# Kernel optimization log

Hardware: AMD Instinct MI355X
Metric: run time of the kernel (lower is better)

## Reference

```python
import jax, jax.numpy as jnp
import numpy as np
from jax.scipy.special import logsumexp

OT_ITER = 8
USE_POSITIVITY = True
LN_EPS = 1e-5
PROB_L = 2
EPS = 1e-4


def _layer_norm(x, w, b):
    mu = jnp.mean(x, axis=-1, keepdims=True)
    var = jnp.mean(jnp.square(x - mu), axis=-1, keepdims=True)
    return (x - mu) * jax.lax.rsqrt(var + LN_EPS) * w + b


def _sinkhorn(attn, log_mu, log_nu):
    # attn: [B, H, W+1, W+1]
    v = log_nu - logsumexp(attn, axis=2)
    u = log_mu - logsumexp(attn + v[:, :, None, :], axis=3)

    def step(uv, _):
        u, v = uv
        v = log_nu - logsumexp(attn + u[..., None], axis=2)
        u = log_mu - logsumexp(attn + v[:, :, None, :], axis=3)
        return (u, v), None

    (u, v), _ = jax.lax.scan(step, (u, v), None, length=OT_ITER - 1)
    return attn + u[..., None] + v[:, :, None, :]


def _optimal_transport(attn):
    w = attn.shape[-1]
    # pad one dustbin row/col with zeros
    attn = jnp.pad(attn, ((0, 0), (0, 0), (0, 1), (0, 1)))
    marginal = jnp.concatenate([jnp.ones((w,), attn.dtype), jnp.full((1,), float(w), attn.dtype)]) / (2.0 * w)
    log_mu = jnp.log(marginal).reshape(1, 1, w + 1)
    log_nu = log_mu
    out = _sinkhorn(attn, log_mu, log_nu)
    return jnp.exp(out[:, :, :-1, :-1] + jnp.log(2.0 * w))


def _forward(feature, ln_weight, ln_bias):
    w = feature.shape[-1]
    x = jnp.transpose(feature, (0, 2, 3, 1))          # [2B, H, W, C]
    x = _layer_norm(x, ln_weight, ln_bias)
    b2 = x.shape[0]
    f0, f1 = x[: b2 // 2], x[b2 // 2:]                 # [B, H, W, C] each

    cv = jnp.einsum('bhic,bhjc->bhij', f0, f1)         # [B, H, W, W]
    # F.interpolate(scale_factor=1/2, mode='nearest') == stride-2 slicing
    f0d, f1d = f0[:, ::2, ::2, :], f1[:, ::2, ::2, :]
    cv_down = jnp.einsum('bhic,bhjc->bhij', f0d, f1d)  # [B, H/2, W/2, W/2]

    if USE_POSITIVITY:
        mask = jnp.triu(jnp.ones((w, w), bool), 1)
    else:
        mask = jnp.zeros((w, w), bool)
    cv_mask = jnp.where(mask, -jnp.inf, cv)

    prob = _optimal_transport(cv_mask)                 # [B, H, W, W]
    masked_prob = jnp.where(mask, 0.0, prob)

    prob_max_ind = jnp.argmax(masked_prob, axis=-1)[..., None]  # [B, H, W, 1]
    mpp = jnp.pad(masked_prob, ((0, 0), (0, 0), (0, 0), (PROB_L, PROB_L)))

    conf = jnp.zeros_like(prob_max_ind, dtype=masked_prob.dtype)
    corr = jnp.zeros_like(conf)
    for idx in range(2 * PROB_L + 1):
        weight = jnp.take_along_axis(mpp, prob_max_ind + idx, axis=-1)
        conf = conf + weight
        corr = corr + weight * (prob_max_ind + idx - PROB_L).astype(weight.dtype)
    corr = (corr + EPS) / (conf + EPS)                 # [B, H, W, 1]

    x_grid = jnp.arange(w, dtype=feature.dtype)
    disparity = (x_grid[None, None, :] - corr[..., 0])[:, None]  # [B, 1, H, W]
    conf_out = conf[..., 0][:, None]                              # [B, 1, H, W]
    occ = jnp.sum(masked_prob, axis=-1)[:, None]                  # [B, 1, H, W]
    return (disparity, conf_out, occ, cv, cv_down)


def setup_inputs() -> dict:
    key = jax.random.key(0)
    k1, k2, k3 = jax.random.split(key, 3)
    feature = jax.random.normal(k1, (8, 128, 80, 256), jnp.float32)  # [2B, C, H, W]
    ln_weight = 1.0 + 0.02 * jax.random.normal(k2, (128,), jnp.float32)
    ln_bias = 0.02 * jax.random.normal(k3, (128,), jnp.float32)
    return {"feature": feature, "ln_weight": ln_weight, "ln_bias": ln_bias}


def reference(feature, ln_weight, ln_bias):
    return _forward(feature, ln_weight, ln_bias)
```

## Files before the change

kernel.cpp:

```cpp
#include <hip/hip_runtime.h>

#define CC 128
#define HH 80
#define WW 256
#define NSL 320
#define TRI2_TOT 36864
#define DISP_OFF 0
#define CONF_OFF 81920
#define OCC_OFF  163840
#define CV_OFF   245760
#define CVD_OFF  21217280
#define NU_C (1.0f/512.0f)
#define MU_C (1.0f/512.0f)
#define ST_N 163840
#define LDSW 40

typedef _Float16 f16;
typedef f16 f16x8 __attribute__((ext_vector_type(8)));
typedef float f32x4 __attribute__((ext_vector_type(4)));

__device__ __forceinline__ int ell_of(int m) { return 4 + (((m + 7) >> 3) << 5); }
__device__ __forceinline__ int S_of(int i) {
  int m = i >> 2;
  int q = (m + 7) >> 3, r = (m + 7) & 7;
  int Q = 16*m + ((q*(q-1)) << 9) + ((r*q) << 7);
  return Q + (i & 3) * ell_of(m);
}

__global__ __launch_bounds__(256)
void ln_stats_kernel(const float* __restrict__ feat, float* __restrict__ stats) {
  __shared__ __align__(16) float4 psum[8][32];
  __shared__ __align__(16) float4 psq[8][32];
  const int t = threadIdx.x;
  const int id = blockIdx.x;
  const int wx = id & 1, bh = id >> 1;
  const int bb = bh / HH, h = bh % HH;
  const int tw = t & 31, tc = t >> 5;
  const float* p = feat + ((size_t)(bb*CC + tc*16)*HH + h)*WW + wx*128 + tw*4;
  float4 s4  = make_float4(0.f, 0.f, 0.f, 0.f);
  float4 s24 = make_float4(0.f, 0.f, 0.f, 0.f);
  #pragma unroll
  for (int cc = 0; cc < 16; ++cc) {
    float4 v = *(const float4*)(p + (size_t)cc*HH*WW);
    s4.x += v.x; s4.y += v.y; s4.z += v.z; s4.w += v.w;
    s24.x = fmaf(v.x, v.x, s24.x); s24.y = fmaf(v.y, v.y, s24.y);
    s24.z = fmaf(v.z, v.z, s24.z); s24.w = fmaf(v.w, v.w, s24.w);
  }
  psum[tc][tw] = s4; psq[tc][tw] = s24;
  __syncthreads();
  if (t < 32) {
    float4 S  = psum[0][t];
    float4 S2 = psq[0][t];
    #pragma unroll
    for (int k = 1; k < 8; ++k) {
      float4 a = psum[k][t], b = psq[k][t];
      S.x += a.x; S.y += a.y; S.z += a.z; S.w += a.w;
      S2.x += b.x; S2.y += b.y; S2.z += b.z; S2.w += b.w;
    }
    float4 mu = make_float4(S.x*(1.f/CC), S.y*(1.f/CC), S.z*(1.f/CC), S.w*(1.f/CC));
    float4 rs;
    rs.x = rsqrtf(fmaf(-mu.x, mu.x, S2.x*(1.f/CC)) + 1e-5f);
    rs.y = rsqrtf(fmaf(-mu.y, mu.y, S2.y*(1.f/CC)) + 1e-5f);
    rs.z = rsqrtf(fmaf(-mu.z, mu.z, S2.z*(1.f/CC)) + 1e-5f);
    rs.w = rsqrtf(fmaf(-mu.w, mu.w, S2.w*(1.f/CC)) + 1e-5f);
    *(float4*)&stats[(size_t)bh*WW + wx*128 + 4*t]        = mu;
    *(float4*)&stats[ST_N + (size_t)bh*WW + wx*128 + 4*t] = rs;
  }
}

__global__ __launch_bounds__(256, 3)
void cv_fused_kernel(const float* __restrict__ feat, const float* __restrict__ stats,
                     const float* __restrict__ lnw, const float* __restrict__ lnb,
                     float* __restrict__ cv_out, float* __restrict__ cvd_out) {
  extern __shared__ unsigned short smu[];
  unsigned short* Ah = smu;
  unsigned short* Al = smu + 5120;
  unsigned short* Bh = smu + 10240;
  unsigned short* Bl = smu + 15360;
  __shared__ __align__(16) float rmean[256];
  __shared__ __align__(16) float rrstd[256];
  __shared__ float lwS[128], lbS[128];
  const int t = threadIdx.x;
  const int P = blockIdx.x;
  if (t < 128) { lwS[t] = lnw[t]; lbS[t] = lnb[t]; }
  const int l = t & 63, w = t >> 6;
  const int wm = w >> 1, wn = w & 1;
  const int fr = l & 15, fg = l >> 4;
  const int row = t & 127, khalf = t >> 7;

  const bool iscv = (P < 4*NSL);
  int zz = 0, i0 = 0, j0 = 0, id = 0, ws = 1;
  size_t baseA, baseB;
  if (iscv) {
    const int x = P & 7, m = P >> 3;
    const int q = m & 3, zhi = m >> 2;
    zz = zhi*8 + x;
    i0 = (q >> 1) * 128; j0 = (q & 1) * 128;
    const int b = zz / HH, h = zz % HH;
    baseA = ((size_t)b*CC*HH + (size_t)h)*WW + i0;
    baseB = ((size_t)(b+4)*CC*HH + (size_t)h)*WW + j0;
    const int isA = (t < 128);
    const int rr_ = isA ? (i0 + t) : (j0 + (t - 128));
    const int bb  = isA ? b : (b + 4);
    const size_t si = ((size_t)bb*HH + h)*WW + rr_;
    rmean[t] = stats[si];
    rrstd[t] = stats[ST_N + si];
  } else {
    id = P - 4*NSL;
    const int b = id / 40, hd = id % 40, h = 2*hd;
    ws = 2;
    baseA = ((size_t)b*CC*HH + (size_t)h)*WW;
    baseB = ((size_t)(b+4)*CC*HH + (size_t)h)*WW;
    const int isA = (t < 128);
    const int rowd = isA ? t : (t - 128);
    const int bb = isA ? b : (b + 4);
    const size_t si = ((size_t)bb*HH + h)*WW + 2*rowd;
    rmean[t] = stats[si];
    rrstd[t] = stats[ST_N + si];
  }

  f32x4 acc[4][4];
  #pragma unroll
  for (int mi = 0; mi < 4; ++mi)
    #pragma unroll
    for (int ni = 0; ni < 4; ++ni)
      acc[mi][ni] = (f32x4){0.f, 0.f, 0.f, 0.f};

  float qa[16], qb[16];
  auto loadC = [&](int kc) {
    const size_t co = (size_t)(kc*32 + khalf*16)*HH*WW + (size_t)(row*ws);
    #pragma unroll
    for (int e = 0; e < 16; ++e) {
      qa[e] = feat[baseA + co + (size_t)e*HH*WW];
      qb[e] = feat[baseB + co + (size_t)e*HH*WW];
    }
  };
  auto storeC = [&](int kc) {
    const float rmA = rmean[row],     rrA = rrstd[row];
    const float rmB = rmean[128+row], rrB = rrstd[128+row];
    f16x8 vah[2], val[2], vbh[2], vbl[2];
    #pragma unroll
    for (int e = 0; e < 16; ++e) {
      const int ch = kc*32 + khalf*16 + e;
      const float lw = lwS[ch], lb = lbS[ch];
      float va = (qa[e] - rmA) * rrA * lw + lb;
      f16 ha = (f16)va;
      vah[e >> 3][e & 7] = ha;
      val[e >> 3][e & 7] = (f16)(va - (float)ha);
      float vb = (qb[e] - rmB) * rrB * lw + lb;
      f16 hb = (f16)vb;
      vbh[e >> 3][e & 7] = hb;
      vbl[e >> 3][e & 7] = (f16)(vb - (float)hb);
    }
    const int off = row*LDSW + khalf*16;
    *(f16x8*)&Ah[off] = vah[0]; *(f16x8*)&Ah[off + 8] = vah[1];
    *(f16x8*)&Al[off] = val[0]; *(f16x8*)&Al[off + 8] = val[1];
    *(f16x8*)&Bh[off] = vbh[0]; *(f16x8*)&Bh[off + 8] = vbh[1];
    *(f16x8*)&Bl[off] = vbl[0]; *(f16x8*)&Bl[off + 8] = vbl[1];
  };
  auto compute = [&]() {
    f16x8 a_h[4], a_l[4];
    #pragma unroll
    for (int mi = 0; mi < 4; ++mi) {
      const int r0 = (wm*64 + mi*16 + fr)*LDSW + fg*8;
      a_h[mi] = *(const f16x8*)&Ah[r0];
      a_l[mi] = *(const f16x8*)&Al[r0];
    }
    #pragma unroll
    for (int ni = 0; ni < 4; ++ni) {
      const int c0 = (wn*64 + ni*16 + fr)*LDSW + fg*8;
      f16x8 b_h = *(const f16x8*)&Bh[c0];
      f16x8 b_l = *(const f16x8*)&Bl[c0];
      #pragma unroll
      for (int mi = 0; mi < 4; ++mi) {
        acc[mi][ni] = __builtin_amdgcn_mfma_f32_16x16x32_f16(a_h[mi], b_h, acc[mi][ni], 0, 0, 0);
        acc[mi][ni] = __builtin_amdgcn_mfma_f32_16x16x32_f16(a_h[mi], b_l, acc[mi][ni], 0, 0, 0);
        acc[mi][ni] = __builtin_amdgcn_mfma_f32_16x16x32_f16(a_l[mi], b_h, acc[mi][ni], 0, 0, 0);
      }
    }
  };

  loadC(0);
  __syncthreads();
  storeC(0);
  for (int kc = 0; kc < 4; ++kc) {
    __syncthreads();
    if (kc < 3) loadC(kc + 1);
    compute();
    __syncthreads();
    if (kc < 3) storeC(kc + 1);
  }

  if (iscv) {
    #pragma unroll
    for (int mi = 0; mi < 4; ++mi)
      #pragma unroll
      for (int ni = 0; ni < 4; ++ni) {
        f32x4 v = acc[mi][ni];
        const int orow = i0 + wm*64 + mi*16 + fg*4;
        const int ocol = j0 + wn*64 + ni*16 + fr;
        size_t ob = ((size_t)zz*256 + orow)*256 + ocol;
        cv_out[ob]       = v[0];
        cv_out[ob + 256] = v[1];
        cv_out[ob + 512] = v[2];
        cv_out[ob + 768] = v[3];
      }
  } else {
    #pragma unroll
    for (int mi = 0; mi < 4; ++mi)
      #pragma unroll
      for (int ni = 0; ni < 4; ++ni) {
        f32x4 v = acc[mi][ni];
        const int orow = wm*64 + mi*16 + fg*4;
        const int ocol = wn*64 + ni*16 + fr;
        size_t ob = ((size_t)id*128 + orow)*128 + ocol;
        cvd_out[ob]       = v[0];
        cvd_out[ob + 128] = v[1];
        cvd_out[ob + 256] = v[2];
        cvd_out[ob + 384] = v[3];
      }
  }
}

__global__ __launch_bounds__(1024)
__attribute__((amdgpu_waves_per_eu(4, 4)))
void sink_kernel(const float* __restrict__ cvg, float* __restrict__ out) {
  extern __shared__ float pE[];
  __shared__ __align__(16) float eu[260];
  __shared__ __align__(16) float ev[260];
  __shared__ __align__(16) float buf[8][256];
  __shared__ float vbS[256];
  __shared__ float redbufU[4], redbufV[4], redbufM[16];
  __shared__ float Msh;
  const int t = threadIdx.x;
  const int z = blockIdx.x;
  const float* cvS = cvg + (size_t)z * 65536;

  const int j   = t & 255;
  const int c   = t >> 8;
  const int jo  = 255 - j;
  const int nbj = (j >> 2) + 1;
  const int bkd = nbj < 32 ? nbj : 32;
  const int nd  = (bkd > c) ? ((bkd - c + 3) >> 2) : 0;
  const int ov  = ((jo >> 2) + 1) - 32;
  const int no  = (ov > c) ? ((ov - c + 3) >> 2) : 0;
  const int nv  = nd + no;
  const int rsR = S_of(j);
  const int rsO = S_of(jo);
  const int coovf = 128 + 4*c - 16*nd;

  if (t >= 512 && t < 768) eu[t - 512] = 1.f;
  if (t == 768) eu[256] = 1.f;
  if (t >= 896 && t < 900) redbufU[t - 896] = 64.f;

  float4 eR[9];
  {
    float mx = 0.f;
    #pragma unroll
    for (int r = 0; r < 9; ++r) {
      const bool isd  = r < nd;
      const bool valq = r < nv;
      const int co  = isd ? (4*c + 16*r) : ((coovf + 16*r) & 255);
      const int row = isd ? j : jo;
      float4 v = make_float4(0.f, 0.f, 0.f, 0.f);
      if (valq) {
        v = *(const float4*)&cvS[row*256 + co];
        if (co     <= row) mx = fmaxf(mx, v.x);
        if (co + 1 <= row) mx = fmaxf(mx, v.y);
        if (co + 2 <= row) mx = fmaxf(mx, v.z);
        if (co + 3 <= row) mx = fmaxf(mx, v.w);
      }
      eR[r] = v;
    }
    #pragma unroll
    for (int mm = 32; mm; mm >>= 1) mx = fmaxf(mx, __shfl_xor(mx, mm, 64));
    if ((t & 63) == 0) redbufM[t >> 6] = mx;
  }
  __syncthreads();
  if (t == 0) {
    float m2 = redbufM[0];
    #pragma unroll
    for (int q = 1; q < 16; ++q) m2 = fmaxf(m2, redbufM[q]);
    Msh = m2;
  }
  __syncthreads();
  const float M = Msh;
  const float enM = __expf(-M);

  #pragma unroll
  for (int r = 0; r < 9; ++r) {
    const bool isd  = r < nd;
    const bool valq = r < nv;
    const int co  = isd ? (4*c + 16*r) : ((coovf + 16*r) & 255);
    const int row = isd ? j : jo;
    const int rs  = isd ? rsR : rsO;
    float4 v = eR[r];
    float4 e;
    e.x = (valq && co     <= row) ? __expf(v.x - M) : 0.f;
    e.y = (valq && co + 1 <= row) ? __expf(v.y - M) : 0.f;
    e.z = (valq && co + 2 <= row) ? __expf(v.z - M) : 0.f;
    e.w = (valq && co + 3 <= row) ? __expf(v.w - M) : 0.f;
    eR[r] = e;
    if (valq) *(float4*)&pE[rs + co] = e;
  }
  __syncthreads();

  const int wv   = __builtin_amdgcn_readfirstlane(t >> 6);
  const int lane = t & 63;
  const int c0A  = 4 * lane;

  for (int it = 0; it < 8; ++it) {
    {
      float4 a = make_float4(0.f, 0.f, 0.f, 0.f);
      #pragma unroll 4
      for (int mq = 0; mq < 16; ++mq) {
        const int i = 16*mq + wv;
        const int rs = S_of(i);
        const float u = eu[i];
        if (lane <= (i >> 2)) {
          float4 e = *(const float4*)&pE[rs + c0A];
          a.x = fmaf(e.x, u, a.x); a.y = fmaf(e.y, u, a.y);
          a.z = fmaf(e.z, u, a.z); a.w = fmaf(e.w, u, a.w);
        }
      }
      if (wv < 8) *(float4*)&buf[wv][c0A] = a;
      __syncthreads();
      if (wv >= 8) {
        float4 p = *(const float4*)&buf[wv - 8][c0A];
        p.x += a.x; p.y += a.y; p.z += a.z; p.w += a.w;
        *(float4*)&buf[wv - 8][c0A] = p;
      }
    }
    __syncthreads();
    if (t < 256) {
      float cj = ((buf[0][t] + buf[1][t]) + (buf[2][t] + buf[3][t]))
               + ((buf[4][t] + buf[5][t]) + (buf[6][t] + buf[7][t]))
               + enM * eu[256];
      float evt = NU_C / cj;
      ev[t] = evt;
      float s = evt;
      #pragma unroll
      for (int mm = 32; mm; mm >>= 1) s += __shfl_xor(s, mm, 64);
      if ((t & 63) == 0) redbufV[t >> 6] = s;
    } else if (t == 960) {
      float S = ((redbufU[0] + redbufU[1]) + (redbufU[2] + redbufU[3])) + eu[256];
      ev[256] = 0.5f / (enM * S);
    }
    __syncthreads();
    {
      float d0=0.f,d1=0.f,d2=0.f,d3=0.f;
      float o0=0.f,o1=0.f,o2=0.f,o3=0.f;
      #pragma unroll
      for (int r = 0; r < 9; ++r) {
        const int co = (r < nd) ? (4*c + 16*r) : ((coovf + 16*r) & 255);
        float4 ev4 = *(const float4*)&ev[co];
        float4 e = eR[r];
        float p0 = e.x*ev4.x, p1 = e.y*ev4.y, p2 = e.z*ev4.z, p3 = e.w*ev4.w;
        if (r < nd) { d0 += p0; d1 += p1; d2 += p2; d3 += p3; }
        else        { o0 += p0; o1 += p1; o2 += p2; o3 += p3; }
      }
      buf[c][j]      = (d0 + d1) + (d2 + d3);
      buf[4 + c][jo] = (o0 + o1) + (o2 + o3);
    }
    __syncthreads();
    if (t < 256) {
      float ri = (((buf[0][t] + buf[1][t]) + (buf[2][t] + buf[3][t]))
                + ((buf[4][t] + buf[5][t]) + (buf[6][t] + buf[7][t])))
               + enM * ev[256];
      float u_ = MU_C / ri;
      eu[t] = u_;
      float s = u_;
      #pragma unroll
      for (int mm = 32; mm; mm >>= 1) s += __shfl_xor(s, mm, 64);
      if ((t & 63) == 0) redbufU[t >> 6] = s;
    } else if (t == 960) {
      float S = ((redbufV[0] + redbufV[1]) + (redbufV[2] + redbufV[3])) + ev[256];
      eu[256] = 0.5f / (enM * S);
    }
    __syncthreads();
  }

  {
    float d0=0.f,d1=0.f,d2=0.f,d3=0.f;
    float o0=0.f,o1=0.f,o2=0.f,o3=0.f;
    float vmd = -1.f, vmo = -1.f;
    int jmd = 1 << 30, jmo = 1 << 30;
    #pragma unroll
    for (int r = 0; r < 9; ++r) {
      const bool isd = r < nd;
      const int co = isd ? (4*c + 16*r) : ((coovf + 16*r) & 255);
      float4 ev4 = *(const float4*)&ev[co];
      float4 e = eR[r];
      float p0 = e.x*ev4.x, p1 = e.y*ev4.y, p2 = e.z*ev4.z, p3 = e.w*ev4.w;
      if (isd) {
        d0 += p0; d1 += p1; d2 += p2; d3 += p3;
        if (p0 > vmd) { vmd = p0; jmd = co;     }
        if (p1 > vmd) { vmd = p1; jmd = co + 1; }
        if (p2 > vmd) { vmd = p2; jmd = co + 2; }
        if (p3 > vmd) { vmd = p3; jmd = co + 3; }
      } else {
        o0 += p0; o1 += p1; o2 += p2; o3 += p3;
        if (p0 > vmo) { vmo = p0; jmo = co;     }
        if (p1 > vmo) { vmo = p1; jmo = co + 1; }
        if (p2 > vmo) { vmo = p2; jmo = co + 2; }
        if (p3 > vmo) { vmo = p3; jmo = co + 3; }
      }
    }
    buf[c][j]      = (d0 + d1) + (d2 + d3);
    buf[4 + c][jo] = (o0 + o1) + (o2 + o3);
    __syncthreads();
    if (t < 256) {
      float occT = (((buf[0][t] + buf[1][t]) + (buf[2][t] + buf[3][t]))
                  + ((buf[4][t] + buf[5][t]) + (buf[6][t] + buf[7][t])));
      out[OCC_OFF + z*256 + t] = occT * eu[t] * 512.f;
    }
    __syncthreads();
    buf[c][j]      = vmd;
    buf[4 + c][jo] = vmo;
    __syncthreads();
    if (t < 256)
      vbS[t] = fmaxf(fmaxf(fmaxf(buf[0][t], buf[1][t]), fmaxf(buf[2][t], buf[3][t])),
                     fmaxf(fmaxf(buf[4][t], buf[5][t]), fmaxf(buf[6][t], buf[7][t])));
    __syncthreads();
    ((int*)buf)[c*256 + j]        = (vmd == vbS[j])  ? jmd : (1 << 30);
    ((int*)buf)[(4 + c)*256 + jo] = (vmo == vbS[jo]) ? jmo : (1 << 30);
    __syncthreads();
    if (t < 256) {
      const int* bi = (const int*)buf;
      int jb = min(min(min(bi[t], bi[256 + t]), min(bi[512 + t], bi[768 + t])),
                   min(min(bi[1024 + t], bi[1280 + t]), min(bi[1536 + t], bi[1792 + t])));
      const int rsT = S_of(t);
      const float sc = eu[t] * 512.f;
      float conf = 0.f, corr = 0.f;
      #pragma unroll
      for (int d = 0; d < 5; ++d) {
        int jp = jb + d - 2;
        float wgt = 0.f;
        if (jp >= 0 && jp <= t) wgt = pE[rsT + jp] * ev[jp] * sc;
        conf += wgt;
        corr = fmaf(wgt, (float)jp, corr);
      }
      corr = (corr + 1e-4f) / (conf + 1e-4f);
      out[DISP_OFF + z*256 + t] = (float)t - corr;
      out[CONF_OFF + z*256 + t] = conf;
    }
  }
}

extern "C" void kernel_launch(void* const* d_in, const int* in_sizes, int n_in,
                              void* d_out, int out_size, void* d_ws, size_t ws_size,
                              hipStream_t stream) {
  (void)in_sizes; (void)n_in; (void)out_size; (void)ws_size;
  const float* feat = (const float*)d_in[0];
  const float* lnw  = (const float*)d_in[1];
  const float* lnb  = (const float*)d_in[2];
  float* out = (float*)d_out;
  float* stats = (float*)d_ws;

  (void)hipFuncSetAttribute((const void*)cv_fused_kernel,
                            hipFuncAttributeMaxDynamicSharedMemorySize, 40960);
  (void)hipFuncSetAttribute((const void*)sink_kernel,
                            hipFuncAttributeMaxDynamicSharedMemorySize, TRI2_TOT*4);

  ln_stats_kernel<<<dim3(2*8*HH), 256, 0, stream>>>(feat, stats);
  cv_fused_kernel<<<dim3(4*NSL + 160), 256, 40960, stream>>>(
      feat, stats, lnw, lnb, out + CV_OFF, out + CVD_OFF);
  sink_kernel<<<dim3(NSL), 1024, TRI2_TOT*4, stream>>>(out + CV_OFF, out);
}
```

Before: 287.3 us.

## Keep column-side exp(cost) in registers for Sinkhorn column sums

Each thread now precomputes, before the Sinkhorn loop, a register-resident set of exponentiated cost entries along its column (paired with a mirrored column for load balance). The per-iteration column reduction becomes a register FMA against u read from LDS. This replaces the strided scan of the packed exp matrix in shared memory and removes one barrier plus the two-stage partial-sum merge. It costs 36 extra float registers per thread and uncoalesced strided global loads of the cost volume during setup.

```diff
diff --git a/kernel.cpp b/kernel.cpp
--- a/kernel.cpp
+++ b/kernel.cpp
@@ -249,6 +249,19 @@
   const int rsO = S_of(jo);
   const int coovf = 128 + 4*c - 16*nd;
 
+  const int mj = j >> 2;
+  int ib0_1, n1, ib0_2, n2;
+  if (j < 128) {
+    ib0_1 = 32 + c; n1 = 8;
+    ib0_2 = 64; n2 = 0;
+  } else {
+    ib0_1 = mj + ((c - mj) & 3);
+    n1 = (ib0_1 <= 63) ? (((63 - ib0_1) >> 2) + 1) : 0;
+    const int mo = 63 - mj;
+    ib0_2 = mo + ((c - mo) & 3);
+    n2 = (ib0_2 <= 31) ? (((31 - ib0_2) >> 2) + 1) : 0;
+  }
+
   if (t >= 512 && t < 768) eu[t - 512] = 1.f;
   if (t == 768) eu[256] = 1.f;
   if (t >= 896 && t < 900) redbufU[t - 896] = 64.f;
@@ -303,33 +316,51 @@
     eR[r] = e;
     if (valq) *(float4*)&pE[rs + co] = e;
   }
+
+  float4 eC[9];
+  #pragma unroll
+  for (int r = 0; r < 9; ++r) {
+    const bool own  = r < n1;
+    const int  rr2  = r - n1;
+    const bool valq = own || (rr2 < n2);
+    const int  ib   = own ? (ib0_1 + 4*r) : (ib0_2 + 4*rr2);
+    const int  colq = own ? j : jo;
+    float4 e = make_float4(0.f, 0.f, 0.f, 0.f);
+    if (valq) {
+      const int ibase = 4 * (ib & 63);
+      if (colq <= ibase    ) e.x = __expf(cvS[(ibase    )*256 + colq] - M);
+      if (colq <= ibase + 1) e.y = __expf(cvS[(ibase + 1)*256 + colq] - M);
+      if (colq <= ibase + 2) e.z = __expf(cvS[(ibase + 2)*256 + colq] - M);
+      if (colq <= ibase + 3) e.w = __expf(cvS[(ibase + 3)*256 + colq] - M);
+    }
+    eC[r] = e;
+  }
   __syncthreads();
-
-  const int wv   = __builtin_amdgcn_readfirstlane(t >> 6);
-  const int lane = t & 63;
-  const int c0A  = 4 * lane;
 
   for (int it = 0; it < 8; ++it) {
     {
-      float4 a = make_float4(0.f, 0.f, 0.f, 0.f);
-      #pragma unroll 4
-      for (int mq = 0; mq < 16; ++mq) {
-        const int i = 16*mq + wv;
-        const int rs = S_of(i);
-        const float u = eu[i];
-        if (lane <= (i >> 2)) {
-          float4 e = *(const float4*)&pE[rs + c0A];
-          a.x = fmaf(e.x, u, a.x); a.y = fmaf(e.y, u, a.y);
-          a.z = fmaf(e.z, u, a.z); a.w = fmaf(e.w, u, a.w);
+      float o0=0.f,o1=0.f,o2=0.f,o3=0.f;
+      float p0=0.f,p1=0.f,p2=0.f,p3=0.f;
+      #pragma unroll
+      for (int r = 0; r < 9; ++r) {
+        const bool own  = r < n1;
+        const int  rr2  = r - n1;
+        const bool valq = own || (rr2 < n2);
+        const int  ib   = own ? (ib0_1 + 4*r) : (ib0_2 + 4*rr2);
+        if (valq) {
+          float4 u4 = *(const float4*)&eu[4 * (ib & 63)];
+          float4 e = eC[r];
+          if (own) {
+            o0 = fmaf(e.x, u4.x, o0); o1 = fmaf(e.y, u4.y, o1);
+            o2 = fmaf(e.z, u4.z, o2); o3 = fmaf(e.w, u4.w, o3);
+          } else {
+            p0 = fmaf(e.x, u4.x, p0); p1 = fmaf(e.y, u4.y, p1);
+            p2 = fmaf(e.z, u4.z, p2); p3 = fmaf(e.w, u4.w, p3);
+          }
         }
       }
-      if (wv < 8) *(float4*)&buf[wv][c0A] = a;
-      __syncthreads();
-      if (wv >= 8) {
-        float4 p = *(const float4*)&buf[wv - 8][c0A];
-        p.x += a.x; p.y += a.y; p.z += a.z; p.w += a.w;
-        *(float4*)&buf[wv - 8][c0A] = p;
-      }
+      buf[c][j]      = (o0 + o1) + (o2 + o3);
+      buf[4 + c][jo] = (p0 + p1) + (p2 + p3);
     }
     __syncthreads();
     if (t < 256) {
```

New measurement: 275.0 us. -4.3%, faster.
